# Kernel tuning notes

Hardware: AMD Instinct MI355X
Metric: run time of the kernel (lower is better)

## Reference

```python
import jax, jax.numpy as jnp
import numpy as np

ALPHA = 1.0  # alpha_max=0.5, current_iter=0: 0.5*(1+cos(0)) = 1.0


def _bbox_map(bboxes, batch_idx, B, H, W, dtype):
    """Vectorized rasterization of [N,4] normalized xywh boxes into per-image
    binary masks [B,1,H,W] (union of boxes per image)."""
    xc, yc, bw, bh = bboxes[:, 0], bboxes[:, 1], bboxes[:, 2], bboxes[:, 3]
    # int() in torch truncates toward zero -> jnp.trunc
    x1 = jnp.maximum(0, jnp.trunc((xc - bw / 2) * W).astype(jnp.int32))
    y1 = jnp.maximum(0, jnp.trunc((yc - bh / 2) * H).astype(jnp.int32))
    x2 = jnp.minimum(W - 1, jnp.trunc((xc + bw / 2) * W).astype(jnp.int32))
    y2 = jnp.minimum(H - 1, jnp.trunc((yc + bh / 2) * H).astype(jnp.int32))
    valid = (x2 > x1) & (y2 > y1)  # [N]
    ys = jnp.arange(H, dtype=jnp.int32)
    xs = jnp.arange(W, dtype=jnp.int32)
    rows = (ys[None, :] >= y1[:, None]) & (ys[None, :] <= y2[:, None])  # [N,H]
    cols = (xs[None, :] >= x1[:, None]) & (xs[None, :] <= x2[:, None])  # [N,W]
    box_mask = (valid[:, None, None] & rows[:, :, None] & cols[:, None, :]).astype(dtype)  # [N,H,W]
    # union of boxes belonging to the same image, clamped to binary
    per_img = jax.ops.segment_sum(box_mask, batch_idx.astype(jnp.int32), num_segments=B)
    return jnp.clip(per_img, 0.0, 1.0)[:, None]  # [B,1,H,W]


def setup_inputs() -> dict:
    key = jax.random.key(0)
    k1, k2, k3 = jax.random.split(key, 3)
    B, C, H, W, N = 16, 256, 128, 128, 320
    x = jax.random.normal(k1, (B, C, H, W), dtype=jnp.float32)
    bboxes = jax.random.uniform(k2, (N, 4), dtype=jnp.float32)  # normalized xywh
    batch_idx = jnp.sort(jax.random.randint(k3, (N,), 0, B)).astype(jnp.int64)
    return {"x": x, "bboxes": bboxes, "batch_idx": batch_idx}


def reference(x, bboxes, batch_idx):
    B, C, H, W = x.shape
    bbox_map = _bbox_map(bboxes, batch_idx, B, H, W, x.dtype)  # [B,1,H,W]
    c_avg = jnp.mean(x, axis=1, keepdims=True)                 # [B,1,H,W]
    return x + ALPHA * bbox_map * c_avg                        # broadcast over C
```

## Files before the change

### kernel.cpp

```cpp
#include <hip/hip_runtime.h>

#define CH      256
#define HH      128
#define WW      128
#define HWPIX   (HH * WW)
#define NTHR    512
#define CPG     16
#define QUADS   32

typedef float nativef4 __attribute__((ext_vector_type(4)));

__global__ __launch_bounds__(NTHR, 4) void k_fused(
    const float* __restrict__ x,
    const float* __restrict__ bboxes,
    const int*   __restrict__ batch_idx,
    float*       __restrict__ out,
    int N)
{
    const int b = blockIdx.x >> 7;
    const int r = blockIdx.x & 127;
    const int q = threadIdx.x & (QUADS - 1);
    const int g = threadIdx.x >> 5;

    const size_t base = ((size_t)b * CH + (size_t)g * CPG) * HWPIX
                      + (size_t)r * WW + 4 * q;
    const float4* __restrict__ xq = (const float4*)(x + base);
    const size_t pstride = HWPIX / 4;

    __shared__ unsigned long long smask[2];
    __shared__ float4 part[CPG][QUADS];

    if (threadIdx.x < 2) smask[threadIdx.x] = 0ull;
    __syncthreads();

    float4 v[CPG];
    #pragma unroll
    for (int j = 0; j < CPG; ++j)
        v[j] = xq[(size_t)j * pstride];

    for (int n = threadIdx.x; n < N; n += NTHR) {
        if (batch_idx[n] != b) continue;
        const float xc = bboxes[4 * n + 0];
        const float yc = bboxes[4 * n + 1];
        const float bw = bboxes[4 * n + 2];
        const float bh = bboxes[4 * n + 3];
        const int x1 = max(0,      (int)truncf((xc - bw * 0.5f) * (float)WW));
        const int y1 = max(0,      (int)truncf((yc - bh * 0.5f) * (float)HH));
        const int x2 = min(WW - 1, (int)truncf((xc + bw * 0.5f) * (float)WW));
        const int y2 = min(HH - 1, (int)truncf((yc + bh * 0.5f) * (float)HH));
        if (!(x2 > x1 && y2 > y1)) continue;
        if (r < y1 || r > y2) continue;
        {
            const int a0 = x1;
            const int b0 = min(x2, 63);
            if (a0 <= b0) {
                const unsigned long long hm =
                    (b0 == 63) ? ~0ull : ((1ull << (b0 + 1)) - 1ull);
                const unsigned long long lm = (1ull << a0) - 1ull;
                atomicOr(&smask[0], hm & ~lm);
            }
        }
        {
            const int a0 = max(x1 - 64, 0);
            const int b0 = x2 - 64;
            if (b0 >= 0 && a0 <= b0) {
                const unsigned long long hm =
                    (b0 == 63) ? ~0ull : ((1ull << (b0 + 1)) - 1ull);
                const unsigned long long lm = (1ull << a0) - 1ull;
                atomicOr(&smask[1], hm & ~lm);
            }
        }
    }

    float4 ps = make_float4(0.f, 0.f, 0.f, 0.f);
    #pragma unroll
    for (int j = 0; j < CPG; ++j) {
        ps.x += v[j].x; ps.y += v[j].y; ps.z += v[j].z; ps.w += v[j].w;
    }
    part[g][q] = ps;
    __syncthreads();

    float4 tot = make_float4(0.f, 0.f, 0.f, 0.f);
    #pragma unroll
    for (int gg = 0; gg < CPG; ++gg) {
        const float4 p = part[gg][q];
        tot.x += p.x; tot.y += p.y; tot.z += p.z; tot.w += p.w;
    }

    const unsigned long long m = smask[q >> 4];
    const int bit0 = (4 * q) & 63;
    const float inv = 1.0f / (float)CH;
    float4 a;
    a.x = ((m >> (bit0 + 0)) & 1ull) ? tot.x * inv : 0.0f;
    a.y = ((m >> (bit0 + 1)) & 1ull) ? tot.y * inv : 0.0f;
    a.z = ((m >> (bit0 + 2)) & 1ull) ? tot.z * inv : 0.0f;
    a.w = ((m >> (bit0 + 3)) & 1ull) ? tot.w * inv : 0.0f;

    nativef4* __restrict__ oq = (nativef4*)(out + base);
    #pragma unroll
    for (int j = 0; j < CPG; ++j) {
        const float4 vv = v[j];
        nativef4 o;
        o.x = vv.x + a.x; o.y = vv.y + a.y; o.z = vv.z + a.z; o.w = vv.w + a.w;
        __builtin_nontemporal_store(o, &oq[(size_t)j * pstride]);
    }
}

extern "C" void kernel_launch(void* const* d_in, const int* in_sizes, int n_in,
                              void* d_out, int out_size, void* d_ws, size_t ws_size,
                              hipStream_t stream)
{
    const float* x         = (const float*)d_in[0];
    const float* bboxes    = (const float*)d_in[1];
    const int*   batch_idx = (const int*)d_in[2];
    float*       out       = (float*)d_out;

    const int N = in_sizes[1] / 4;
    const int B = 16;

    const int blocks = B * HH;
    k_fused<<<blocks, NTHR, 0, stream>>>(x, bboxes, batch_idx, out, N);
}
```

Measured before the change: 84.66 us.

## Process two rows per block with 32 channels per thread group

Each block now covers a 256-pixel tile (two rows) using 8 groups of 64 threads, and each thread holds 32 channels in registers instead of 16. This halves the block count, halves the per-block bbox scan and the shared-memory partial-sum reduction work per pixel, and builds separate masks for the two rows. In exchange, register pressure doubles (launch bounds lowered to 2 blocks per SM), which lowers occupancy and may reduce latency hiding on this memory-bound kernel.

```diff
diff --git a/kernel.cpp b/kernel.cpp
--- a/kernel.cpp
+++ b/kernel.cpp
@@ -5,32 +5,36 @@
 #define WW      128
 #define HWPIX   (HH * WW)
 #define NTHR    512
-#define CPG     16
-#define QUADS   32
+#define NGRP    8
+#define CPG     32
+#define TILE_PX 256
 
 typedef float nativef4 __attribute__((ext_vector_type(4)));
 
-__global__ __launch_bounds__(NTHR, 4) void k_fused(
+__global__ __launch_bounds__(NTHR, 2) void k_fused(
     const float* __restrict__ x,
     const float* __restrict__ bboxes,
     const int*   __restrict__ batch_idx,
     float*       __restrict__ out,
     int N)
 {
-    const int b = blockIdx.x >> 7;
-    const int r = blockIdx.x & 127;
-    const int q = threadIdx.x & (QUADS - 1);
-    const int g = threadIdx.x >> 5;
+    const int b    = blockIdx.x >> 6;
+    const int tile = blockIdx.x & 63;
+    const int pix0 = tile * TILE_PX;
+    const int r0   = tile * 2;
+
+    const int q = threadIdx.x & 63;
+    const int g = threadIdx.x >> 6;
 
     const size_t base = ((size_t)b * CH + (size_t)g * CPG) * HWPIX
-                      + (size_t)r * WW + 4 * q;
+                      + pix0 + 4 * q;
     const float4* __restrict__ xq = (const float4*)(x + base);
     const size_t pstride = HWPIX / 4;
 
-    __shared__ unsigned long long smask[2];
-    __shared__ float4 part[CPG][QUADS];
+    __shared__ unsigned long long smask[4];
+    __shared__ float4 part[NGRP][64];
 
-    if (threadIdx.x < 2) smask[threadIdx.x] = 0ull;
+    if (threadIdx.x < 4) smask[threadIdx.x] = 0ull;
     __syncthreads();
 
     float4 v[CPG];
@@ -49,7 +53,9 @@
         const int x2 = min(WW - 1, (int)truncf((xc + bw * 0.5f) * (float)WW));
         const int y2 = min(HH - 1, (int)truncf((yc + bh * 0.5f) * (float)HH));
         if (!(x2 > x1 && y2 > y1)) continue;
-        if (r < y1 || r > y2) continue;
+        if (y2 < r0 || y1 > r0 + 1) continue;
+
+        unsigned long long m0 = 0ull, m1 = 0ull;
         {
             const int a0 = x1;
             const int b0 = min(x2, 63);
@@ -57,7 +63,7 @@
                 const unsigned long long hm =
                     (b0 == 63) ? ~0ull : ((1ull << (b0 + 1)) - 1ull);
                 const unsigned long long lm = (1ull << a0) - 1ull;
-                atomicOr(&smask[0], hm & ~lm);
+                m0 = hm & ~lm;
             }
         }
         {
@@ -67,27 +73,39 @@
                 const unsigned long long hm =
                     (b0 == 63) ? ~0ull : ((1ull << (b0 + 1)) - 1ull);
                 const unsigned long long lm = (1ull << a0) - 1ull;
-                atomicOr(&smask[1], hm & ~lm);
+                m1 = hm & ~lm;
             }
+        }
+        if (r0 >= y1 && r0 <= y2) {
+            if (m0) atomicOr(&smask[0], m0);
+            if (m1) atomicOr(&smask[1], m1);
+        }
+        if (r0 + 1 >= y1 && r0 + 1 <= y2) {
+            if (m0) atomicOr(&smask[2], m0);
+            if (m1) atomicOr(&smask[3], m1);
         }
     }
 
-    float4 ps = make_float4(0.f, 0.f, 0.f, 0.f);
+    float4 s0 = make_float4(0.f, 0.f, 0.f, 0.f);
+    float4 s1 = make_float4(0.f, 0.f, 0.f, 0.f);
     #pragma unroll
-    for (int j = 0; j < CPG; ++j) {
-        ps.x += v[j].x; ps.y += v[j].y; ps.z += v[j].z; ps.w += v[j].w;
+    for (int j = 0; j < CPG; j += 2) {
+        s0.x += v[j].x;     s0.y += v[j].y;     s0.z += v[j].z;     s0.w += v[j].w;
+        s1.x += v[j + 1].x; s1.y += v[j + 1].y; s1.z += v[j + 1].z; s1.w += v[j + 1].w;
     }
-    part[g][q] = ps;
+    s0.x += s1.x; s0.y += s1.y; s0.z += s1.z; s0.w += s1.w;
+
+    part[g][q] = s0;
     __syncthreads();
 
     float4 tot = make_float4(0.f, 0.f, 0.f, 0.f);
     #pragma unroll
-    for (int gg = 0; gg < CPG; ++gg) {
+    for (int gg = 0; gg < NGRP; ++gg) {
         const float4 p = part[gg][q];
         tot.x += p.x; tot.y += p.y; tot.z += p.z; tot.w += p.w;
     }
 
-    const unsigned long long m = smask[q >> 4];
+    const unsigned long long m = smask[2 * (q >> 5) + ((q >> 4) & 1)];
     const int bit0 = (4 * q) & 63;
     const float inv = 1.0f / (float)CH;
     float4 a;
@@ -118,6 +136,6 @@
     const int N = in_sizes[1] / 4;
     const int B = 16;
 
-    const int blocks = B * HH;
+    const int blocks = B * (HWPIX / TILE_PX);
     k_fused<<<blocks, NTHR, 0, stream>>>(x, bboxes, batch_idx, out, N);
 }
```

New measurement: 89.33 us. +5.5%, slower.

## Split each row into two half-width tiles with fewer channels per thread

Applied to the files above, without the earlier changes.

Each block now covers half an image row (64 pixels) instead of a full row, so there are twice as many blocks. Threads hold 8 channels instead of 16, and 32 channel groups are reduced through shared memory. This halves per-thread register use to allow more resident blocks (launch bounds 8) and more memory parallelism. In exchange the box-mask loop runs twice as often in total and each row segment is 256 B instead of 512 B.

```diff
diff --git a/kernel.cpp b/kernel.cpp
--- a/kernel.cpp
+++ b/kernel.cpp
@@ -5,32 +5,36 @@
 #define WW      128
 #define HWPIX   (HH * WW)
 #define NTHR    512
-#define CPG     16
-#define QUADS   32
+#define NGRP    32
+#define CPG     8
+#define QUADS   16
 
 typedef float nativef4 __attribute__((ext_vector_type(4)));
 
-__global__ __launch_bounds__(NTHR, 4) void k_fused(
+__global__ __launch_bounds__(NTHR, 8) void k_fused(
     const float* __restrict__ x,
     const float* __restrict__ bboxes,
     const int*   __restrict__ batch_idx,
     float*       __restrict__ out,
     int N)
 {
-    const int b = blockIdx.x >> 7;
-    const int r = blockIdx.x & 127;
+    const int b     = blockIdx.x >> 8;
+    const int tile  = blockIdx.x & 255;
+    const int r     = tile >> 1;
+    const int wbase = (tile & 1) << 6;
+
     const int q = threadIdx.x & (QUADS - 1);
-    const int g = threadIdx.x >> 5;
+    const int g = threadIdx.x >> 4;
 
     const size_t base = ((size_t)b * CH + (size_t)g * CPG) * HWPIX
-                      + (size_t)r * WW + 4 * q;
+                      + (size_t)r * WW + wbase + 4 * q;
     const float4* __restrict__ xq = (const float4*)(x + base);
     const size_t pstride = HWPIX / 4;
 
-    __shared__ unsigned long long smask[2];
-    __shared__ float4 part[CPG][QUADS];
+    __shared__ unsigned long long smask;
+    __shared__ float4 part[NGRP][QUADS];
 
-    if (threadIdx.x < 2) smask[threadIdx.x] = 0ull;
+    if (threadIdx.x == 0) smask = 0ull;
     __syncthreads();
 
     float4 v[CPG];
@@ -50,26 +54,13 @@
         const int y2 = min(HH - 1, (int)truncf((yc + bh * 0.5f) * (float)HH));
         if (!(x2 > x1 && y2 > y1)) continue;
         if (r < y1 || r > y2) continue;
-        {
-            const int a0 = x1;
-            const int b0 = min(x2, 63);
-            if (a0 <= b0) {
-                const unsigned long long hm =
-                    (b0 == 63) ? ~0ull : ((1ull << (b0 + 1)) - 1ull);
-                const unsigned long long lm = (1ull << a0) - 1ull;
-                atomicOr(&smask[0], hm & ~lm);
-            }
-        }
-        {
-            const int a0 = max(x1 - 64, 0);
-            const int b0 = x2 - 64;
-            if (b0 >= 0 && a0 <= b0) {
-                const unsigned long long hm =
-                    (b0 == 63) ? ~0ull : ((1ull << (b0 + 1)) - 1ull);
-                const unsigned long long lm = (1ull << a0) - 1ull;
-                atomicOr(&smask[1], hm & ~lm);
-            }
-        }
+        const int a0 = max(x1 - wbase, 0);
+        const int b0 = min(x2 - wbase, 63);
+        if (a0 > b0) continue;
+        const unsigned long long hm =
+            (b0 == 63) ? ~0ull : ((1ull << (b0 + 1)) - 1ull);
+        const unsigned long long lm = (1ull << a0) - 1ull;
+        atomicOr(&smask, hm & ~lm);
     }
 
     float4 ps = make_float4(0.f, 0.f, 0.f, 0.f);
@@ -82,13 +73,13 @@
 
     float4 tot = make_float4(0.f, 0.f, 0.f, 0.f);
     #pragma unroll
-    for (int gg = 0; gg < CPG; ++gg) {
+    for (int gg = 0; gg < NGRP; ++gg) {
         const float4 p = part[gg][q];
         tot.x += p.x; tot.y += p.y; tot.z += p.z; tot.w += p.w;
     }
 
-    const unsigned long long m = smask[q >> 4];
-    const int bit0 = (4 * q) & 63;
+    const unsigned long long m = smask;
+    const int bit0 = 4 * q;
     const float inv = 1.0f / (float)CH;
     float4 a;
     a.x = ((m >> (bit0 + 0)) & 1ull) ? tot.x * inv : 0.0f;
@@ -118,6 +109,6 @@
     const int N = in_sizes[1] / 4;
     const int B = 16;
 
-    const int blocks = B * HH;
+    const int blocks = B * 256;
     k_fused<<<blocks, NTHR, 0, stream>>>(x, bboxes, batch_idx, out, N);
 }
```

Result: faster. 81.67 us (median of 2 runs) (-3.5%).
